# Kernel tuning notes

Hardware: AMD Instinct MI355X
Metric: run time of the kernel (lower is better)

The kernel has to match this reference:

```python
import jax, jax.numpy as jnp
import numpy as np

# Performer config (from module __init__):
# dim=768, depth=4, heads=12, dim_head=64, nb_features=64,
# generalized_attention=True with ReLU kernel, reversible=True,
# ff_mult=4, shift_tokens=True (shifts=(-1,0,1) since causal=False),
# qkv_bias=True, attn_out_bias=True, ff_chunks=1, dropout=0.
L, D, H, DH, M = 4, 768, 12, 64, 64
FF = 4 * D
SHIFTS = (-1, 0, 1)
KERNEL_EPS = 1e-3


def _layer_norm(x, g, b, eps=1e-5):
    mu = jnp.mean(x, axis=-1, keepdims=True)
    var = jnp.mean((x - mu) ** 2, axis=-1, keepdims=True)
    return (x - mu) / jnp.sqrt(var + eps) * g + b


def _shift(t, amount, mask=None):
    # F.pad(t, (0,0, amount, -amount)): pad front by amount, trim end (or vice versa)
    if amount == 0:
        return t
    if mask is not None:
        t = jnp.where(mask[..., None], t, jnp.zeros((), t.dtype))
    S = t.shape[1]
    f, bk = max(amount, 0), max(-amount, 0)
    return jnp.pad(t, ((0, 0), (f, bk), (0, 0)))[:, bk:bk + S]


def _shift_tokens(x, mask=None):
    # PreShiftTokens with shifts=(-1,0,1): split channels into 3 chunks, shift each along seq
    n = len(SHIFTS)
    fps = x.shape[-1] // n
    parts = [_shift(x[..., i * fps:(i + 1) * fps], a, mask) for i, a in enumerate(SHIFTS)]
    rest = x[..., n * fps:]
    if rest.shape[-1]:
        parts.append(rest)
    return jnp.concatenate(parts, axis=-1)


def _attn(x, mask, Wq, bq, Wk, bk, Wv, bv, Wo, bo, g, bl, P):
    # PreShiftTokens(mask-aware) -> PreLayerNorm -> SelfAttention (FAVOR+ generalized ReLU kernel)
    x = _shift_tokens(x, mask)
    h = _layer_norm(x, g, bl)
    B, S, _ = h.shape
    heads = lambda t: t.reshape(B, S, H, DH).transpose(0, 2, 1, 3)  # b h s d
    q = heads(h @ Wq + bq)
    k = heads(h @ Wk + bk)
    v = heads(h @ Wv + bv)
    # library semantics: zero v where mask is False (module passes input_ids.eq(0))
    v = jnp.where(mask[:, None, :, None], v, jnp.zeros((), v.dtype))
    dn = DH ** -0.25  # data_normalizer
    qp = jax.nn.relu(jnp.einsum('bhnd,md->bhnm', q * dn, P)) + KERNEL_EPS  # [B,H,S,M]
    kp = jax.nn.relu(jnp.einsum('bhnd,md->bhnm', k * dn, P)) + KERNEL_EPS
    ks = kp.sum(axis=2)                                   # [B,H,M]
    d_inv = 1.0 / jnp.einsum('bhnm,bhm->bhn', qp, ks)     # [B,H,S]
    ctx = jnp.einsum('bhnm,bhnd->bhmd', kp, v)            # [B,H,M,DH]
    out = jnp.einsum('bhmd,bhnm,bhn->bhnd', ctx, qp, d_inv)
    out = out.transpose(0, 2, 1, 3).reshape(B, S, H * DH)
    return out @ Wo + bo


def _ff(x, g, bl, W1, b1, W2, b2):
    # PreShiftTokens (no mask routed to FF) -> PreLayerNorm -> FeedForward (exact GELU)
    x = _shift_tokens(x, None)
    h = _layer_norm(x, g, bl)
    return jax.nn.gelu(h @ W1 + b1, approximate=False) @ W2 + b2


def _forward(x, Wq, bq, Wk, bk, Wv, bv, Wo, bo, ln1_g, ln1_b, W1, b1, W2, b2, ln2_g, ln2_b, proj, input_ids):
    mask = (input_ids == 0)  # structure != 'hi': src_pad_mask = input_ids.eq(0)
    # ReversibleSequence: x -> (x, x); per block: y1 = x1 + attn(x2), y2 = x2 + ff(y1)
    x1, x2 = x, x
    for l in range(L):
        y1 = x1 + _attn(x2, mask, Wq[l], bq[l], Wk[l], bk[l], Wv[l], bv[l],
                        Wo[l], bo[l], ln1_g[l], ln1_b[l], proj[l])
        y2 = x2 + _ff(y1, ln2_g[l], ln2_b[l], W1[l], b1[l], W2[l], b2[l])
        x1, x2 = y1, y2
    return (x1 + x2) * 0.5  # stack(chunk(2)).mean(0)


def setup_inputs() -> dict:
    key = jax.random.key(0)
    ks = jax.random.split(key, 16)
    B, S = 8, 2048
    s = 0.02
    f32 = jnp.float32
    return {
        'x': jax.random.normal(ks[0], (B, S, D), f32),
        'input_ids': jax.random.randint(ks[1], (B, S), 0, 1000, dtype=jnp.int32),
        'Wq': jax.random.normal(ks[2], (L, D, D), f32) * s,
        'bq': jnp.zeros((L, D), f32),
        'Wk': jax.random.normal(ks[3], (L, D, D), f32) * s,
        'bk': jnp.zeros((L, D), f32),
        'Wv': jax.random.normal(ks[4], (L, D, D), f32) * s,
        'bv': jnp.zeros((L, D), f32),
        'Wo': jax.random.normal(ks[5], (L, D, D), f32) * s,
        'bo': jnp.zeros((L, D), f32),
        'ln1_g': jnp.ones((L, D), f32),
        'ln1_b': jnp.zeros((L, D), f32),
        'W1': jax.random.normal(ks[6], (L, D, FF), f32) * s,
        'b1': jnp.zeros((L, FF), f32),
        'W2': jax.random.normal(ks[7], (L, FF, D), f32) * s,
        'b2': jnp.zeros((L, D), f32),
        'ln2_g': jnp.ones((L, D), f32),
        'ln2_b': jnp.zeros((L, D), f32),
        'proj': jax.random.normal(ks[8], (L, M, DH), f32),  # FAVOR+ random projection per layer
    }


def reference(x, Wq, bq, Wk, bk, Wv, bv, Wo, bo, ln1_g, ln1_b, W1, b1, W2, b2, ln2_g, ln2_b, proj, input_ids):
    return _forward(x, Wq, bq, Wk, bk, Wv, bv, Wo, bo, ln1_g, ln1_b,
                    W1, b1, W2, b2, ln2_g, ln2_b, proj, input_ids)
```

## Files before the change

kernel.cpp:

```cpp
#include <hip/hip_runtime.h>
#include <cstdint>
#include <cstddef>

typedef __bf16 bf16_t;
typedef bf16_t bf16x4 __attribute__((ext_vector_type(4)));
typedef bf16_t bf16x8 __attribute__((ext_vector_type(8)));
typedef float  f32x4  __attribute__((ext_vector_type(4)));

#define LAYERS 4
#define DMODEL 768
#define NHEAD  12
#define DHEAD  64
#define MFEAT  64
#define FFDIM  3072
#define BB     8
#define SSEQ   2048
#define BSROWS (BB*SSEQ)
#define QROWS  (BSROWS*NHEAD)
#define FFCHUNK (BSROWS/2)
#define SCH    16
#define SPC    (SSEQ/SCH)
#define NBH    (BB*NHEAD)

__device__ __forceinline__ void gload_lds16(const bf16_t* g, bf16_t* l) {
    __builtin_amdgcn_global_load_lds(
        (const __attribute__((address_space(1))) uint32_t*)g,
        (__attribute__((address_space(3))) uint32_t*)l, 16, 0, 0);
}

__global__ __launch_bounds__(256) void castT_kernel(
    const float* __restrict__ in, bf16_t* __restrict__ out, int K, int N)
{
    __shared__ float t[32][33];
    int kb = blockIdx.x * 32, nb = blockIdx.y * 32;
    int tx = threadIdx.x & 31, ty = threadIdx.x >> 5;
#pragma unroll
    for (int i = 0; i < 32; i += 8)
        t[ty + i][tx] = in[(size_t)(kb + ty + i) * N + nb + tx];
    __syncthreads();
#pragma unroll
    for (int i = 0; i < 32; i += 8)
        out[(size_t)(nb + ty + i) * K + kb + tx] = (bf16_t)t[tx][ty + i];
}

__global__ __launch_bounds__(256) void castP_kernel(
    const float* __restrict__ in, bf16_t* __restrict__ out)
{
    int i = blockIdx.x * 256 + threadIdx.x;
    out[i] = (bf16_t)(in[i] * 0.3535533905932738f);
}

__global__ __launch_bounds__(256) void biascat_kernel(
    const float* __restrict__ bq, const float* __restrict__ bk,
    const float* __restrict__ bv, float* __restrict__ out)
{
    int i = blockIdx.x * 256 + threadIdx.x;
    int l = i / 2304, j = i % 2304;
    float v = (j < 768) ? bq[l * 768 + j]
            : (j < 1536) ? bk[l * 768 + j - 768]
                         : bv[l * 768 + j - 1536];
    out[i] = v;
}

template<bool MASKED>
__global__ __launch_bounds__(256) void shiftln_kernel(
    const float* __restrict__ x, const int* __restrict__ ids,
    const float* __restrict__ g, const float* __restrict__ bl,
    bf16_t* __restrict__ out)
{
    const int r = blockIdx.x;
    const int b = r >> 11;
    const int s = r & 2047;
    const int tid = threadIdx.x;
    float v0, v1, v2;
    {
        int s2 = s + 1;
        bool ok = (s2 < SSEQ) && (!MASKED || ids[b * SSEQ + s2] == 0);
        v0 = ok ? x[((size_t)(b * SSEQ + s2)) * DMODEL + tid] : 0.f;
    }
    v1 = x[((size_t)r) * DMODEL + tid + 256];
    {
        int s2 = s - 1;
        bool ok = (s2 >= 0) && (!MASKED || ids[b * SSEQ + s2] == 0);
        v2 = ok ? x[((size_t)(b * SSEQ + s2)) * DMODEL + tid + 512] : 0.f;
    }
    float sum = v0 + v1 + v2;
    float sq  = v0 * v0 + v1 * v1 + v2 * v2;
#pragma unroll
    for (int off = 32; off; off >>= 1) {
        sum += __shfl_down(sum, off);
        sq  += __shfl_down(sq, off);
    }
    __shared__ float red[2][4];
    int lane = tid & 63, w = tid >> 6;
    if (lane == 0) { red[0][w] = sum; red[1][w] = sq; }
    __syncthreads();
    sum = red[0][0] + red[0][1] + red[0][2] + red[0][3];
    sq  = red[1][0] + red[1][1] + red[1][2] + red[1][3];
    float mu  = sum * (1.f / DMODEL);
    float var = sq * (1.f / DMODEL) - mu * mu;
    float rstd = rsqrtf(var + 1e-5f);
    size_t base = (size_t)r * DMODEL;
    out[base + tid]       = (bf16_t)((v0 - mu) * rstd * g[tid]       + bl[tid]);
    out[base + tid + 256] = (bf16_t)((v1 - mu) * rstd * g[tid + 256] + bl[tid + 256]);
    out[base + tid + 512] = (bf16_t)((v2 - mu) * rstd * g[tid + 512] + bl[tid + 512]);
}

template<int BM, int BN, int EPI>
__global__ __launch_bounds__(256) void gemm_kernel(
    const bf16_t* __restrict__ A, const bf16_t* __restrict__ Bt,
    const float* __restrict__ bias, const float* resid,
    const int* __restrict__ ids, void* outp,
    int N, int K)
{
    constexpr int BK = 64;
    constexpr int WM = BM / 2, WN = BN / 2;
    constexpr int AM = WM / 16, AN = WN / 16;
    __shared__ bf16_t As[2][BM * BK];
    __shared__ bf16_t Bs[2][BN * BK];
    const int tid  = threadIdx.x;
    const int lane = tid & 63, wid = tid >> 6;
    const int wr = wid >> 1, wc = wid & 1;
    const int gx = gridDim.x;
    const int nwg = gx * (int)gridDim.y;
    int orig = (int)blockIdx.y * gx + (int)blockIdx.x;
    int wgid = orig;
    if ((nwg & 7) == 0) wgid = (orig & 7) * (nwg >> 3) + (orig >> 3);
    const int rowBase = (wgid / gx) * BM;
    const int colBase = (wgid % gx) * BN;

    f32x4 acc[AM][AN];
#pragma unroll
    for (int i = 0; i < AM; i++)
#pragma unroll
        for (int j = 0; j < AN; j++) { f32x4 z = {0.f,0.f,0.f,0.f}; acc[i][j] = z; }

    const int rl = lane & 15;
    const int c0 = lane >> 4;
    const int sx = rl & 7;

    auto stage = [&](int t, int buf) {
        const int k0 = t * BK;
#pragma unroll
        for (int i = 0; i < (BM * 8) / 256; i++) {
            int idx = i * 256 + tid;
            int row = idx >> 3, ccp = idx & 7;
            int ccl = ccp ^ (row & 7);
            gload_lds16(&A[(size_t)(rowBase + row) * K + k0 + ccl * 8],
                        &As[buf][idx * 8]);
        }
#pragma unroll
        for (int i = 0; i < (BN * 8) / 256; i++) {
            int idx = i * 256 + tid;
            int row = idx >> 3, ccp = idx & 7;
            int ccl = ccp ^ (row & 7);
            gload_lds16(&Bt[(size_t)(colBase + row) * K + k0 + ccl * 8],
                        &Bs[buf][idx * 8]);
        }
    };

    const int NT = K / BK;
    stage(0, 0);
    __syncthreads();
    int cur = 0;
    for (int t = 0; t < NT; t++) {
        if (t + 1 < NT) stage(t + 1, cur ^ 1);
#pragma unroll
        for (int kk = 0; kk < 2; kk++) {
            const int ccp = ((kk << 2) | c0) ^ sx;
            bf16x8 af[AM], bfr[AN];
#pragma unroll
            for (int i = 0; i < AM; i++)
                af[i] = *(const bf16x8*)&As[cur][(wr * WM + i * 16 + rl) * BK + ccp * 8];
#pragma unroll
            for (int j = 0; j < AN; j++)
                bfr[j] = *(const bf16x8*)&Bs[cur][(wc * WN + j * 16 + rl) * BK + ccp * 8];
#pragma unroll
            for (int i = 0; i < AM; i++)
#pragma unroll
                for (int j = 0; j < AN; j++)
                    acc[i][j] = __builtin_amdgcn_mfma_f32_16x16x32_bf16(
                        af[i], bfr[j], acc[i][j], 0, 0, 0);
        }
        __syncthreads();
        cur ^= 1;
    }

#pragma unroll
    for (int i = 0; i < AM; i++)
#pragma unroll
        for (int j = 0; j < AN; j++) {
            int col = colBase + wc * WN + j * 16 + rl;
#pragma unroll
            for (int r4 = 0; r4 < 4; r4++) {
                int row = rowBase + wr * WM + i * 16 + (lane >> 4) * 4 + r4;
                float v = acc[i][j][r4];
                if constexpr (EPI == 2) {
                    float o = v > 0.f ? v : 0.f;
                    ((bf16_t*)outp)[(size_t)row * N + col] = (bf16_t)(o + 0.001f);
                } else if constexpr (EPI == 3) {
                    float xg = v + bias[col];
                    float o = 0.5f * xg * (1.f + erff(xg * 0.70710678118654752f));
                    ((bf16_t*)outp)[(size_t)row * N + col] = (bf16_t)o;
                } else if constexpr (EPI == 4) {
                    size_t idx = (size_t)row * N + col;
                    ((float*)outp)[idx] = v + bias[col] + resid[idx];
                } else {
                    int third = col / DMODEL;
                    int colq  = col - third * DMODEL;
                    float o = v + bias[col];
                    if (third == 2 && ids[row] != 0) o = 0.f;
                    bf16_t* ob = (bf16_t*)outp + (size_t)third * BSROWS * DMODEL;
                    ob[(size_t)row * DMODEL + colq] = (bf16_t)o;
                }
            }
        }
}

__global__ __launch_bounds__(256) void ctx_partial_kernel(
    const bf16_t* __restrict__ kp, const bf16_t* __restrict__ v,
    float* __restrict__ part, float* __restrict__ ksp)
{
    const int blk = blockIdx.x;
    const int bh = blk / SCH, chunk = blk % SCH;
    const int b = bh / NHEAD, h = bh % NHEAD;
    __shared__ float kpf[SPC][64];
    __shared__ float vf[SPC][64];
    const int tid = threadIdx.x;
#pragma unroll
    for (int i = 0; i < 4; i++) {
        int idx = tid + i * 256;
        int sl = idx >> 3, c = (idx & 7) * 8;
        size_t go = ((size_t)(b * SSEQ + chunk * SPC + sl) * NHEAD + h) * 64 + c;
        bf16x8 kv8 = *(const bf16x8*)&kp[go];
        bf16x8 vv8 = *(const bf16x8*)&v[go];
#pragma unroll
        for (int e = 0; e < 8; e++) {
            kpf[sl][c + e] = (float)kv8[e];
            vf[sl][c + e]  = (float)vv8[e];
        }
    }
    __syncthreads();
    const int m = tid & 63, dg = tid >> 6;
    float ksacc = 0.f;
    f32x4 acc[4];
#pragma unroll
    for (int jg = 0; jg < 4; jg++) { f32x4 z = {0.f,0.f,0.f,0.f}; acc[jg] = z; }
    for (int sl = 0; sl < SPC; sl++) {
        float kv = kpf[sl][m];
        ksacc += kv;
#pragma unroll
        for (int jg = 0; jg < 4; jg++) {
            f32x4 c4 = *(const f32x4*)&vf[sl][dg * 16 + jg * 4];
            acc[jg] += kv * c4;
        }
    }
    size_t obase = ((size_t)chunk * NBH + bh) * 4096 + (size_t)m * 64 + dg * 16;
#pragma unroll
    for (int jg = 0; jg < 4; jg++)
#pragma unroll
        for (int e = 0; e < 4; e++) part[obase + jg * 4 + e] = acc[jg][e];
    if (dg == 0) ksp[((size_t)chunk * NBH + bh) * 64 + m] = ksacc;
}

__global__ __launch_bounds__(256) void ctx_reduce_kernel(
    const float* __restrict__ part, float* __restrict__ ctxb)
{
    int e = blockIdx.x * 256 + threadIdx.x;
    float s = 0.f;
#pragma unroll
    for (int c = 0; c < SCH; c++) s += part[(size_t)c * NBH * 4096 + e];
    ctxb[e] = s;
}

__global__ __launch_bounds__(256) void attnout_kernel(
    const bf16_t* __restrict__ qp, const float* __restrict__ ctx,
    const float* __restrict__ ksp, bf16_t* __restrict__ out)
{
    const int blk = blockIdx.x;
    const int sc = blk & 31;
    const int bh = blk >> 5;
    const int b = bh / NHEAD, h = bh % NHEAD;
    __shared__ float ctxs[64][64];
    __shared__ float kss[64];
    const int tid = threadIdx.x;
#pragma unroll
    for (int i = 0; i < 16; i++) {
        int flat = tid + i * 256;
        ctxs[flat >> 6][flat & 63] = ctx[(size_t)bh * 4096 + flat];
    }
    if (tid < 64) {
        float s = 0.f;
#pragma unroll
        for (int c = 0; c < SCH; c++) s += ksp[((size_t)c * NBH + bh) * 64 + tid];
        kss[tid] = s;
    }
    __syncthreads();
    const int sl = tid >> 2, dg = tid & 3;
    const int s = sc * 64 + sl;
    const bf16_t* qrow = &qp[((size_t)(b * SSEQ + s) * NHEAD + h) * 64];
    float den = 0.f;
    f32x4 acc[4];
#pragma unroll
    for (int jg = 0; jg < 4; jg++) { f32x4 z = {0.f,0.f,0.f,0.f}; acc[jg] = z; }
#pragma unroll 4
    for (int m = 0; m < 64; m++) {
        float qv = (float)qrow[m];
        den += qv * kss[m];
#pragma unroll
        for (int jg = 0; jg < 4; jg++) {
            f32x4 c4 = *(const f32x4*)&ctxs[m][dg * 16 + jg * 4];
            acc[jg] += qv * c4;
        }
    }
    float inv = 1.f / den;
    size_t obase = (size_t)(b * SSEQ + s) * DMODEL + h * 64 + dg * 16;
#pragma unroll
    for (int jg = 0; jg < 4; jg++)
#pragma unroll
        for (int e = 0; e < 4; e++)
            out[obase + jg * 4 + e] = (bf16_t)(acc[jg][e] * inv);
}

__global__ void avg_kernel(const float* __restrict__ a, const float* __restrict__ b,
                           float* __restrict__ o, int n4)
{
    for (int i = blockIdx.x * 256 + threadIdx.x; i < n4; i += gridDim.x * 256) {
        f32x4 av = ((const f32x4*)a)[i];
        f32x4 bv = ((const f32x4*)b)[i];
        ((f32x4*)o)[i] = (av + bv) * 0.5f;
    }
}

extern "C" void kernel_launch(void* const* d_in, const int* in_sizes, int n_in,
                              void* d_out, int out_size, void* d_ws, size_t ws_size,
                              hipStream_t stream)
{
    int idi = 1, base = 2;
    if (in_sizes[1] != BSROWS) { idi = n_in - 1; base = 1; }
    const float* x_f   = (const float*)d_in[0];
    const int*   ids   = (const int*)d_in[idi];
    const float* Wq    = (const float*)d_in[base + 0];
    const float* bq    = (const float*)d_in[base + 1];
    const float* Wk    = (const float*)d_in[base + 2];
    const float* bk    = (const float*)d_in[base + 3];
    const float* Wv    = (const float*)d_in[base + 4];
    const float* bv    = (const float*)d_in[base + 5];
    const float* Wo    = (const float*)d_in[base + 6];
    const float* bo    = (const float*)d_in[base + 7];
    const float* ln1g  = (const float*)d_in[base + 8];
    const float* ln1b  = (const float*)d_in[base + 9];
    const float* W1    = (const float*)d_in[base + 10];
    const float* b1    = (const float*)d_in[base + 11];
    const float* W2    = (const float*)d_in[base + 12];
    const float* b2    = (const float*)d_in[base + 13];
    const float* ln2g  = (const float*)d_in[base + 14];
    const float* ln2b  = (const float*)d_in[base + 15];
    const float* proj  = (const float*)d_in[base + 16];

    char* p = (char*)d_ws;
    auto alloc = [&](size_t bytes) -> char* {
        char* r = p; p += (bytes + 255) & ~(size_t)255; return r;
    };
    float*  r1   = (float*)d_out;
    float*  r2   = (float*)alloc((size_t)BSROWS * DMODEL * 4);
    bf16_t* hbuf = (bf16_t*)alloc((size_t)BSROWS * DMODEL * 2);
    char*   ub   = alloc((size_t)3 * BSROWS * DMODEL * 2);
    bf16_t* qb   = (bf16_t*)ub;
    bf16_t* kb   = (bf16_t*)(ub + (size_t)BSROWS * DMODEL * 2);
    bf16_t* vb   = (bf16_t*)(ub + (size_t)2 * BSROWS * DMODEL * 2);
    bf16_t* gff  = (bf16_t*)ub;
    float*  ctxb = (float*)alloc((size_t)NBH * 64 * 64 * 4);
    float*  ksp  = (float*)alloc((size_t)SCH * NBH * 64 * 4);
    char*   wu   = alloc((size_t)2 * DMODEL * FFDIM * 2);
    bf16_t* wqkvt = (bf16_t*)wu;
    bf16_t* wot  = (bf16_t*)(wu + (size_t)3 * DMODEL * DMODEL * 2);
    bf16_t* w1t  = (bf16_t*)wu;
    bf16_t* w2t  = (bf16_t*)(wu + (size_t)DMODEL * FFDIM * 2);
    bf16_t* pb   = (bf16_t*)alloc((size_t)MFEAT * DHEAD * 2);
    float*  bqkv = (float*)alloc((size_t)LAYERS * 2304 * 4);
    float*  ctxpart = (float*)hbuf;

    biascat_kernel<<<(LAYERS * 2304) / 256, 256, 0, stream>>>(bq, bk, bv, bqkv);

    const float* c1 = x_f;
    const float* c2 = x_f;

    for (int l = 0; l < LAYERS; l++) {
        castT_kernel<<<dim3(24, 24), 256, 0, stream>>>(Wq + (size_t)l * DMODEL * DMODEL, wqkvt, DMODEL, DMODEL);
        castT_kernel<<<dim3(24, 24), 256, 0, stream>>>(Wk + (size_t)l * DMODEL * DMODEL, wqkvt + (size_t)DMODEL * DMODEL, DMODEL, DMODEL);
        castT_kernel<<<dim3(24, 24), 256, 0, stream>>>(Wv + (size_t)l * DMODEL * DMODEL, wqkvt + (size_t)2 * DMODEL * DMODEL, DMODEL, DMODEL);
        castT_kernel<<<dim3(24, 24), 256, 0, stream>>>(Wo + (size_t)l * DMODEL * DMODEL, wot, DMODEL, DMODEL);
        castP_kernel<<<16, 256, 0, stream>>>(proj + (size_t)l * MFEAT * DHEAD, pb);

        shiftln_kernel<true><<<BSROWS, 256, 0, stream>>>(
            c2, ids, ln1g + l * DMODEL, ln1b + l * DMODEL, hbuf);
        gemm_kernel<128, 128, 5><<<dim3(2304 / 128, BSROWS / 128), 256, 0, stream>>>(
            hbuf, wqkvt, bqkv + l * 2304, nullptr, ids, qb, 2304, DMODEL);
        gemm_kernel<128, 64, 2><<<dim3(1, QROWS / 128), 256, 0, stream>>>(
            qb, pb, nullptr, nullptr, nullptr, qb, MFEAT, DHEAD);
        gemm_kernel<128, 64, 2><<<dim3(1, QROWS / 128), 256, 0, stream>>>(
            kb, pb, nullptr, nullptr, nullptr, kb, MFEAT, DHEAD);
        ctx_partial_kernel<<<NBH * SCH, 256, 0, stream>>>(kb, vb, ctxpart, ksp);
        ctx_reduce_kernel<<<(NBH * 4096) / 256, 256, 0, stream>>>(ctxpart, ctxb);
        attnout_kernel<<<NBH * (SSEQ / 64), 256, 0, stream>>>(qb, ctxb, ksp, hbuf);
        gemm_kernel<128, 128, 4><<<dim3(DMODEL / 128, BSROWS / 128), 256, 0, stream>>>(
            hbuf, wot, bo + l * DMODEL, c1, nullptr, r1, DMODEL, DMODEL);
        c1 = r1;

        castT_kernel<<<dim3(24, 96), 256, 0, stream>>>(W1 + (size_t)l * DMODEL * FFDIM, w1t, DMODEL, FFDIM);
        castT_kernel<<<dim3(96, 24), 256, 0, stream>>>(W2 + (size_t)l * FFDIM * DMODEL, w2t, FFDIM, DMODEL);

        shiftln_kernel<false><<<BSROWS, 256, 0, stream>>>(
            c1, ids, ln2g + l * DMODEL, ln2b + l * DMODEL, hbuf);
        for (int ch = 0; ch < 2; ch++) {
            const bf16_t* hA = hbuf + (size_t)ch * FFCHUNK * DMODEL;
            gemm_kernel<128, 128, 3><<<dim3(FFDIM / 128, FFCHUNK / 128), 256, 0, stream>>>(
                hA, w1t, b1 + l * FFDIM, nullptr, nullptr, gff, FFDIM, DMODEL);
            gemm_kernel<128, 128, 4><<<dim3(DMODEL / 128, FFCHUNK / 128), 256, 0, stream>>>(
                gff, w2t, b2 + l * DMODEL, c2 + (size_t)ch * FFCHUNK * DMODEL, nullptr,
                r2 + (size_t)ch * FFCHUNK * DMODEL, DMODEL, FFDIM);
        }
        c2 = r2;
    }

    avg_kernel<<<4096, 256, 0, stream>>>(c1, c2, (float*)d_out,
                                         (BSROWS * DMODEL) / 4);
}
```

Before: 2.545 ms.

## Add 256x256-tile 8-wave GEMM for QKV and FF1 projections

Adds a new 512-thread GEMM kernel with 256x256 output tiles, double-buffered LDS with XOR swizzling, and an XCD-aware workgroup remapping. It also interleaves the next tile's global-to-LDS staging with MFMA quadrants and uses s_setprio around the MFMA blocks. The kernel is used for the QKV projection and the first FF matmul. Larger tiles raise arithmetic intensity and cut global traffic, at the cost of 128 KB of LDS per block, which limits occupancy to one block per CU, and fewer blocks in flight.

```diff
diff --git a/kernel.cpp b/kernel.cpp
--- a/kernel.cpp
+++ b/kernel.cpp
@@ -217,6 +217,123 @@
         }
 }
 
+template<int EPI>
+__global__ __launch_bounds__(512) void gemm8_kernel(
+    const bf16_t* __restrict__ A, const bf16_t* __restrict__ Bt,
+    const float* __restrict__ bias, const int* __restrict__ ids,
+    void* outp, int N, int K)
+{
+    __shared__ bf16_t As[2][256 * 64];
+    __shared__ bf16_t Bs[2][256 * 64];
+    const int tid  = threadIdx.x;
+    const int lane = tid & 63, wid = tid >> 6;
+    const int wr = wid >> 2, wc = wid & 3;
+    const int gx = gridDim.x;
+    const int nwg = gx * (int)gridDim.y;
+    int orig = (int)blockIdx.y * gx + (int)blockIdx.x;
+    int wgid = orig;
+    if ((nwg & 7) == 0) wgid = (orig & 7) * (nwg >> 3) + (orig >> 3);
+    const int rowBase = (wgid / gx) * 256;
+    const int colBase = (wgid % gx) * 256;
+
+    f32x4 acc[8][4];
+#pragma unroll
+    for (int i = 0; i < 8; i++)
+#pragma unroll
+        for (int j = 0; j < 4; j++) { f32x4 z = {0.f,0.f,0.f,0.f}; acc[i][j] = z; }
+
+    const int rl = lane & 15;
+    const int c0 = lane >> 4;
+    const int sx = rl & 7;
+
+    auto stage_kt = [&](int kt, int buf) {
+        const int k0 = kt * 64;
+#pragma unroll
+        for (int i = 0; i < 4; i++) {
+            int idx = i * 512 + tid;
+            int row = idx >> 3, ccp = idx & 7;
+            int ccl = ccp ^ (row & 7);
+            gload_lds16(&A[(size_t)(rowBase + row) * K + k0 + ccl * 8],
+                        &As[buf][idx * 8]);
+        }
+#pragma unroll
+        for (int i = 0; i < 4; i++) {
+            int idx = i * 512 + tid;
+            int row = idx >> 3, ccp = idx & 7;
+            int ccl = ccp ^ (row & 7);
+            gload_lds16(&Bt[(size_t)(colBase + row) * K + k0 + ccl * 8],
+                        &Bs[buf][idx * 8]);
+        }
+    };
+
+    const int NKT = K / 64;
+    stage_kt(0, 0);
+    asm volatile("s_waitcnt vmcnt(0)" ::: "memory");
+    __builtin_amdgcn_s_barrier();
+
+    for (int u = 0; u < NKT; u++) {
+        const int buf = u & 1;
+#pragma unroll
+        for (int qd = 0; qd < 4; qd++) {
+            const int ri0 = (qd >> 1) * 4, cj0 = (qd & 1) * 2;
+            bf16x8 af[2][4], bfr[2][2];
+#pragma unroll
+            for (int kk = 0; kk < 2; kk++) {
+                const int ccp = ((kk << 2) | c0) ^ sx;
+#pragma unroll
+                for (int ii = 0; ii < 4; ii++)
+                    af[kk][ii] = *(const bf16x8*)
+                        &As[buf][(wr * 128 + (ri0 + ii) * 16 + rl) * 64 + ccp * 8];
+#pragma unroll
+                for (int jj = 0; jj < 2; jj++)
+                    bfr[kk][jj] = *(const bf16x8*)
+                        &Bs[buf][(wc * 64 + (cj0 + jj) * 16 + rl) * 64 + ccp * 8];
+            }
+            if (qd == 0 && u + 1 < NKT) stage_kt(u + 1, buf ^ 1);
+            __builtin_amdgcn_s_barrier();
+            __builtin_amdgcn_s_setprio(1);
+#pragma unroll
+            for (int kk = 0; kk < 2; kk++)
+#pragma unroll
+                for (int ii = 0; ii < 4; ii++)
+#pragma unroll
+                    for (int jj = 0; jj < 2; jj++)
+                        acc[ri0 + ii][cj0 + jj] =
+                            __builtin_amdgcn_mfma_f32_16x16x32_bf16(
+                                af[kk][ii], bfr[kk][jj],
+                                acc[ri0 + ii][cj0 + jj], 0, 0, 0);
+            __builtin_amdgcn_s_setprio(0);
+            if (qd == 3) asm volatile("s_waitcnt vmcnt(0)" ::: "memory");
+            asm volatile("s_waitcnt lgkmcnt(0)" ::: "memory");
+            __builtin_amdgcn_s_barrier();
+        }
+    }
+
+#pragma unroll
+    for (int i = 0; i < 8; i++)
+#pragma unroll
+        for (int j = 0; j < 4; j++) {
+            int col = colBase + wc * 64 + j * 16 + rl;
+#pragma unroll
+            for (int r4 = 0; r4 < 4; r4++) {
+                int row = rowBase + wr * 128 + i * 16 + (lane >> 4) * 4 + r4;
+                float v = acc[i][j][r4];
+                if constexpr (EPI == 3) {
+                    float xg = v + bias[col];
+                    float o = 0.5f * xg * (1.f + erff(xg * 0.70710678118654752f));
+                    ((bf16_t*)outp)[(size_t)row * N + col] = (bf16_t)o;
+                } else {
+                    int third = col / DMODEL;
+                    int colq  = col - third * DMODEL;
+                    float o = v + bias[col];
+                    if (third == 2 && ids[row] != 0) o = 0.f;
+                    bf16_t* ob = (bf16_t*)outp + (size_t)third * BSROWS * DMODEL;
+                    ob[(size_t)row * DMODEL + colq] = (bf16_t)o;
+                }
+            }
+        }
+}
+
 __global__ __launch_bounds__(256) void ctx_partial_kernel(
     const bf16_t* __restrict__ kp, const bf16_t* __restrict__ v,
     float* __restrict__ part, float* __restrict__ ksp)
@@ -395,8 +512,8 @@
 
         shiftln_kernel<true><<<BSROWS, 256, 0, stream>>>(
             c2, ids, ln1g + l * DMODEL, ln1b + l * DMODEL, hbuf);
-        gemm_kernel<128, 128, 5><<<dim3(2304 / 128, BSROWS / 128), 256, 0, stream>>>(
-            hbuf, wqkvt, bqkv + l * 2304, nullptr, ids, qb, 2304, DMODEL);
+        gemm8_kernel<5><<<dim3(2304 / 256, BSROWS / 256), 512, 0, stream>>>(
+            hbuf, wqkvt, bqkv + l * 2304, ids, qb, 2304, DMODEL);
         gemm_kernel<128, 64, 2><<<dim3(1, QROWS / 128), 256, 0, stream>>>(
             qb, pb, nullptr, nullptr, nullptr, qb, MFEAT, DHEAD);
         gemm_kernel<128, 64, 2><<<dim3(1, QROWS / 128), 256, 0, stream>>>(
@@ -415,8 +532,8 @@
             c1, ids, ln2g + l * DMODEL, ln2b + l * DMODEL, hbuf);
         for (int ch = 0; ch < 2; ch++) {
             const bf16_t* hA = hbuf + (size_t)ch * FFCHUNK * DMODEL;
-            gemm_kernel<128, 128, 3><<<dim3(FFDIM / 128, FFCHUNK / 128), 256, 0, stream>>>(
-                hA, w1t, b1 + l * FFDIM, nullptr, nullptr, gff, FFDIM, DMODEL);
+            gemm8_kernel<3><<<dim3(FFDIM / 256, FFCHUNK / 256), 512, 0, stream>>>(
+                hA, w1t, b1 + l * FFDIM, nullptr, gff, FFDIM, DMODEL);
             gemm_kernel<128, 128, 4><<<dim3(DMODEL / 128, FFCHUNK / 128), 256, 0, stream>>>(
                 gff, w2t, b2 + l * DMODEL, c2 + (size_t)ch * FFCHUNK * DMODEL, nullptr,
                 r2 + (size_t)ch * FFCHUNK * DMODEL, DMODEL, FFDIM);
```

Measured after the change: 2.756 ms. +8.3%, slower.
